# Kernel optimization log

Measured on AMD Instinct MI355X. Metric: run time of the kernel, lower is better.

## Reference

```python
import jax, jax.numpy as jnp
import numpy as np

B, N, D = 1, 4301, 768          # batch, tokens (4200 patch + 1 cls + 100 det), dim
H, HD = 12, 64                  # heads, head_dim (all_head_dim = 768)
NDET = 100                      # det tokens at the end of the sequence
EPS = 1e-5                      # torch LayerNorm default eps
SCALE = HD ** -0.5


def setup_inputs() -> dict:
    key = jax.random.key(0)
    ks = jax.random.split(key, 10)
    w = lambda k: jax.random.normal(k, (D, D), dtype=jnp.float32) * 0.02
    return {
        "x": jax.random.normal(ks[0], (B, N, D), dtype=jnp.float32),
        "wq_p": w(ks[1]), "wk_p": w(ks[2]), "wv_p": w(ks[3]),
        "wq_d": w(ks[4]), "wk_d": w(ks[5]), "wv_d": w(ks[6]),
        "bq_p": jnp.zeros((D,), jnp.float32), "bv_p": jnp.zeros((D,), jnp.float32),
        "bq_d": jnp.zeros((D,), jnp.float32), "bv_d": jnp.zeros((D,), jnp.float32),
        "ln_g": jnp.ones((D,), jnp.float32), "ln_b": jnp.zeros((D,), jnp.float32),
        "wo_p": w(ks[7]), "bo_p": jnp.zeros((D,), jnp.float32),
        "wo_d": w(ks[8]), "bo_d": jnp.zeros((D,), jnp.float32),
    }


def reference(x, wq_p, wk_p, wv_p, wq_d, wk_d, wv_d,
              bq_p, bv_p, bq_d, bv_d, ln_g, ln_b,
              wo_p, bo_p, wo_d, bo_d):
    xp = x[:, :-NDET, :]                       # [B, N-100, D] patch (+cls) tokens
    xd = x[:, -NDET:, :]                       # [B, 100, D]   det tokens
    # separate patch/det QKV projections (subln=True path; k has no bias)
    q = jnp.concatenate([xp @ wq_p.T + bq_p, xd @ wq_d.T + bq_d], axis=1)
    k = jnp.concatenate([xp @ wk_p.T,        xd @ wk_d.T],        axis=1)
    v = jnp.concatenate([xp @ wv_p.T + bv_p, xd @ wv_d.T + bv_d], axis=1)
    split = lambda t: t.reshape(B, N, H, HD).transpose(0, 2, 1, 3)  # [B,H,N,HD]
    q, k, v = split(q) * SCALE, split(k), split(v)
    # unfused attention (memory_efficient_attention_pytorch, attn_mask=None)
    attn = jax.nn.softmax(jnp.einsum("bhqd,bhkd->bhqk", q, k), axis=-1)
    o = jnp.einsum("bhqk,bhkd->bhqd", attn, v)
    o = o.transpose(0, 2, 1, 3).reshape(B, N, D)
    # inner_attn_ln (LayerNorm over all_head_dim)
    mu = o.mean(-1, keepdims=True)
    var = ((o - mu) ** 2).mean(-1, keepdims=True)
    o = (o - mu) * jax.lax.rsqrt(var + EPS) * ln_g + ln_b
    # separate patch/det output projections
    out = jnp.concatenate([o[:, :-NDET, :] @ wo_p.T + bo_p,
                           o[:, -NDET:, :] @ wo_d.T + bo_d], axis=1)
    return out
```

## Files before the change

kernel.cpp:

```cpp
#include <hip/hip_runtime.h>
#include <hip/hip_bf16.h>

#define NT 4301
#define NP 4201
#define NDET 100
#define DMODEL 768
#define NHEAD 12
#define HD 64
#define LN_EPS 1e-5f
#define LOG2E 1.4426950408889634f
#define QSCALE (0.125f * LOG2E)
#define NTP 4352
#define NCHUNK 68
#define FRAGSZ 512
#define CHUNKSZ 4096

typedef __hip_bfloat16 bf16;
typedef __attribute__((ext_vector_type(4))) float f32x4;
typedef __attribute__((ext_vector_type(8))) short frag8;
typedef __attribute__((ext_vector_type(2))) unsigned int u32x2;

static __device__ __forceinline__ void permlane32_swap(unsigned& a, unsigned& b) {
#if __has_builtin(__builtin_amdgcn_permlane32_swap)
    u32x2 r = __builtin_amdgcn_permlane32_swap(a, b, false, false);
    a = r[0]; b = r[1];
#else
    asm("v_permlane32_swap_b32 %0, %1" : "+v"(a), "+v"(b));
#endif
}
static __device__ __forceinline__ void permlane16_swap(unsigned& a, unsigned& b) {
#if __has_builtin(__builtin_amdgcn_permlane16_swap)
    u32x2 r = __builtin_amdgcn_permlane16_swap(a, b, false, false);
    a = r[0]; b = r[1];
#else
    asm("v_permlane16_swap_b32 %0, %1" : "+v"(a), "+v"(b));
#endif
}

static __device__ __forceinline__ unsigned pack_bf16_rh(float a, float b) {
    unsigned ua = __builtin_bit_cast(unsigned, a) + 0x8000u;
    unsigned ub = __builtin_bit_cast(unsigned, b) + 0x8000u;
    return __builtin_amdgcn_perm(ub, ua, 0x07060302u);
}

static __device__ __forceinline__ void gload16(const bf16* g, bf16* l) {
    __builtin_amdgcn_global_load_lds(
        (const __attribute__((address_space(1))) void*)g,
        (__attribute__((address_space(3))) void*)l, 16, 0, 0);
}

__global__ __launch_bounds__(256) void cast_all_kernel(
    const float* __restrict__ x,
    const float* __restrict__ w0, const float* __restrict__ w1,
    const float* __restrict__ w2, const float* __restrict__ w3,
    const float* __restrict__ w4, const float* __restrict__ w5,
    const float* __restrict__ w6, const float* __restrict__ w7,
    bf16* __restrict__ dst, int nx, int nw, int total) {
    int i4 = (blockIdx.x * 256 + threadIdx.x) * 4;
    if (i4 >= total) return;
    const float* s;
    int off;
    if (i4 < nx) {
        s = x; off = i4;
    } else {
        int r = i4 - nx;
        int w = r / nw;
        off = r - w * nw;
        s = w0;
        if (w == 1) s = w1; else if (w == 2) s = w2; else if (w == 3) s = w3;
        else if (w == 4) s = w4; else if (w == 5) s = w5;
        else if (w == 6) s = w6; else if (w == 7) s = w7;
    }
    float4 v = *(const float4*)(s + off);
    bf16 o[4] = {__float2bfloat16(v.x), __float2bfloat16(v.y),
                 __float2bfloat16(v.z), __float2bfloat16(v.w)};
    *(ushort4*)(dst + i4) = *(ushort4*)o;
}

__global__ __launch_bounds__(256, 4) void qkv_kernel(
    const bf16* __restrict__ xb, const bf16* __restrict__ wbase,
    const float* __restrict__ bq_p, const float* __restrict__ bq_d,
    const float* __restrict__ bv_p, const float* __restrict__ bv_d,
    bf16* __restrict__ Qb, bf16* __restrict__ Ksw, bf16* __restrict__ Vsw) {
    __shared__ bf16 As[64][32];
    __shared__ bf16 Bs[192][32];

    const int tid = threadIdx.x;
    const int wave = tid >> 6, lane = tid & 63;
    const int quad = lane >> 4, l16 = lane & 15;
    const int bx = blockIdx.x;
    const int h = blockIdx.y;
    const int is_det = bx >= 66;
    const int row0 = is_det ? NP + (bx - 66) * 64 : bx * 64;
    const int Mlim = is_det ? NT : NP;
    const int col0 = h * 64;
    const size_t nw = (size_t)DMODEL * DMODEL;
    const bf16* W = wbase + (is_det ? 3 * nw : 0);

    const f32x4 z4 = {0.f, 0.f, 0.f, 0.f};
    f32x4 acc[4][3];
#pragma unroll
    for (int r4 = 0; r4 < 4; ++r4)
#pragma unroll
        for (int f = 0; f < 3; ++f) acc[r4][f] = z4;

    const int srow = tid >> 2;
    const int scol8 = (tid & 3) * 8;
    int a_r = row0 + srow;
    if (a_r >= Mlim) a_r = Mlim - 1;
    const bf16* ap = xb + (size_t)a_r * DMODEL + scol8;
    const bf16* bp = W + (size_t)(col0 + srow) * DMODEL + scol8;

    uint4 areg  = *(const uint4*)(ap);
    uint4 breg0 = *(const uint4*)(bp);
    uint4 breg1 = *(const uint4*)(bp + nw);
    uint4 breg2 = *(const uint4*)(bp + 2 * nw);

    for (int k0 = 0; k0 < DMODEL; k0 += 32) {
        __syncthreads();
        *(uint4*)(&As[srow][scol8]) = areg;
        *(uint4*)(&Bs[srow][scol8]) = breg0;
        *(uint4*)(&Bs[64 + srow][scol8]) = breg1;
        *(uint4*)(&Bs[128 + srow][scol8]) = breg2;
        if (k0 + 32 < DMODEL) {
            areg  = *(const uint4*)(ap + k0 + 32);
            breg0 = *(const uint4*)(bp + k0 + 32);
            breg1 = *(const uint4*)(bp + nw + k0 + 32);
            breg2 = *(const uint4*)(bp + 2 * nw + k0 + 32);
        }
        __asm__ volatile("s_waitcnt lgkmcnt(0)" ::: "memory");
        __builtin_amdgcn_s_barrier();
        __asm__ volatile("" ::: "memory");
        frag8 af[4], bfr[3];
#pragma unroll
        for (int r4 = 0; r4 < 4; ++r4)
            af[r4] = *(const frag8*)(&As[r4 * 16 + l16][quad * 8]);
#pragma unroll
        for (int f = 0; f < 3; ++f)
            bfr[f] = *(const frag8*)(&Bs[wave * 48 + f * 16 + l16][quad * 8]);
#pragma unroll
        for (int r4 = 0; r4 < 4; ++r4)
#pragma unroll
            for (int f = 0; f < 3; ++f)
                acc[r4][f] = __builtin_amdgcn_mfma_f32_16x16x32_bf16(af[r4], bfr[f], acc[r4][f], 0, 0, 0);
        __asm__ volatile("" ::: "memory");
    }

#pragma unroll
    for (int f = 0; f < 3; ++f) {
        const int oc = 3 * wave + f;
        const int opi = oc >> 2;
        const int cin = (oc & 3) * 16 + l16;
        const int c = col0 + cin;
        float bv = 0.f, scale = 1.f;
        if (opi == 0) { bv = (is_det ? bq_d : bq_p)[c]; scale = QSCALE; }
        else if (opi == 2) { bv = (is_det ? bv_d : bv_p)[c]; }
#pragma unroll
        for (int r4 = 0; r4 < 4; ++r4) {
#pragma unroll
            for (int j = 0; j < 4; ++j) {
                const int r = row0 + r4 * 16 + quad * 4 + j;
                if (r >= Mlim) continue;
                const bf16 val = __float2bfloat16((acc[r4][f][j] + bv) * scale);
                if (opi == 0) {
                    Qb[(size_t)r * DMODEL + c] = val;
                } else if (opi == 1) {
                    const int cc = r >> 6, tf = (r >> 4) & 3, ln = r & 15;
                    const int s = cin >> 5, qd = (cin >> 3) & 3, je = cin & 7;
                    Ksw[((size_t)(h * NCHUNK + cc) * 8 + tf * 2 + s) * FRAGSZ +
                        (qd * 16 + ln) * 8 + je] = val;
                } else {
                    const int t = cin >> 4, le = cin & 15;
                    const int cc = r >> 6, rr = r & 63;
                    const int sv = rr >> 5, qv = (rr >> 3) & 3, je = rr & 7;
                    Vsw[((size_t)(h * NCHUNK + cc) * 8 + t * 2 + sv) * FRAGSZ +
                        (qv * 16 + le) * 8 + je] = val;
                }
            }
        }
    }
}

__global__ __launch_bounds__(256, 2) void attn_kernel(
    const bf16* __restrict__ Q, const bf16* __restrict__ Ksw,
    const bf16* __restrict__ Vsw, float* __restrict__ O_part,
    float* __restrict__ l_part, int cpb) {
    __shared__ bf16 KV[2][16][FRAGSZ];

    const int tid = threadIdx.x;
    const int wave = tid >> 6, lane = tid & 63;
    const int quad = lane >> 4, l16 = lane & 15;

    int bx, h, z;
    {
        const int id = blockIdx.x;
        const int nblk = gridDim.x;
        const int per = nblk >> 3;
        if ((nblk & 7) == 0 && per % 34 == 0) {
            const int ppx = per / 34;
            const int q = id >> 3;
            const int pair = (id & 7) * ppx + q / 34;
            bx = q % 34;
            h = pair % NHEAD; z = pair / NHEAD;
        } else {
            bx = id % 34; h = (id / 34) % NHEAD; z = id / (34 * NHEAD);
        }
    }
    const int qbase = bx * 128;
    const int hoff = h * HD;
    const int c0 = z * cpb, c1 = c0 + cpb;

    frag8 ones;
#pragma unroll
    for (int j = 0; j < 8; ++j) ones[j] = (short)0x3F80;

    frag8 qf[2][2];
#pragma unroll
    for (int g = 0; g < 2; ++g) {
        int qr = qbase + wave * 32 + g * 16 + l16;
        if (qr >= NT) qr = NT - 1;
#pragma unroll
        for (int s = 0; s < 2; ++s)
            qf[g][s] = *(const frag8*)(Q + (size_t)qr * DMODEL + hoff + s * 32 + quad * 8);
    }

    const bf16* kb0 = Ksw + (size_t)h * NCHUNK * CHUNKSZ + lane * 8;
    const bf16* vb0 = Vsw + (size_t)h * NCHUNK * CHUNKSZ + lane * 8;
    const bf16* sb = (wave < 2) ? kb0 : vb0;
    const int foff = (wave & 1) * 4;
    const int fbase = 4 * wave;

    const f32x4 z4 = {0.f, 0.f, 0.f, 0.f};
    f32x4 accO[2][4], accL[2];
#pragma unroll
    for (int g = 0; g < 2; ++g) {
        accL[g] = z4;
#pragma unroll
        for (int t = 0; t < 4; ++t) accO[g][t] = z4;
    }

    __asm__ volatile("s_waitcnt vmcnt(0)" ::: "memory");

    {
        const bf16* s = sb + (size_t)c0 * CHUNKSZ + foff * FRAGSZ;
#pragma unroll
        for (int i = 0; i < 4; ++i)
            gload16(s + i * FRAGSZ, &KV[0][fbase + i][0]);
    }

    int p = 0;
    for (int c = c0; c < c1; ++c) {
        if (c + 1 < c1) {
            const bf16* s = sb + (size_t)(c + 1) * CHUNKSZ + foff * FRAGSZ;
#pragma unroll
            for (int i = 0; i < 4; ++i)
                gload16(s + i * FRAGSZ, &KV[p ^ 1][fbase + i][0]);
            __asm__ volatile("s_waitcnt vmcnt(4)" ::: "memory");
        } else {
            __asm__ volatile("s_waitcnt vmcnt(0)" ::: "memory");
        }
        __builtin_amdgcn_s_barrier();
        __asm__ volatile("" ::: "memory");

        frag8 kf[8], vf[8];
#pragma unroll
        for (int f = 0; f < 8; ++f) {
            kf[f] = *(const frag8*)(&KV[p][f][lane * 8]);
            vf[f] = *(const frag8*)(&KV[p][8 + f][lane * 8]);
        }

        f32x4 S[2][4];
#pragma unroll
        for (int g = 0; g < 2; ++g)
#pragma unroll
            for (int t = 0; t < 4; ++t) {
                f32x4 s0 = __builtin_amdgcn_mfma_f32_16x16x32_bf16(kf[t * 2 + 0], qf[g][0], z4, 0, 0, 0);
                S[g][t]  = __builtin_amdgcn_mfma_f32_16x16x32_bf16(kf[t * 2 + 1], qf[g][1], s0, 0, 0, 0);
            }
        if (c == NCHUNK - 1) {
            const int kb = c * 64 + quad * 4;
#pragma unroll
            for (int t = 0; t < 4; ++t)
#pragma unroll
                for (int j = 0; j < 4; ++j)
                    if (kb + t * 16 + j >= NT) {
                        S[0][t][j] = -1e30f;
                        S[1][t][j] = -1e30f;
                    }
        }

#pragma unroll
        for (int g = 0; g < 2; ++g) {
            unsigned lo[4], hi[4];
#pragma unroll
            for (int t = 0; t < 4; ++t) {
                lo[t] = pack_bf16_rh(__builtin_exp2f(S[g][t][0]),
                                     __builtin_exp2f(S[g][t][1]));
                hi[t] = pack_bf16_rh(__builtin_exp2f(S[g][t][2]),
                                     __builtin_exp2f(S[g][t][3]));
            }
#pragma unroll
            for (int s = 0; s < 2; ++s) {
                unsigned A = lo[2 * s], B = hi[2 * s];
                unsigned C = lo[2 * s + 1], D = hi[2 * s + 1];
                permlane32_swap(A, C);
                permlane32_swap(B, D);
                permlane16_swap(A, C);
                permlane16_swap(B, D);
                union { unsigned u[4]; frag8 f; } pu;
                pu.u[0] = A; pu.u[1] = B; pu.u[2] = C; pu.u[3] = D;
                const frag8 pf = pu.f;
                accL[g] = __builtin_amdgcn_mfma_f32_16x16x32_bf16(pf, ones, accL[g], 0, 0, 0);
#pragma unroll
                for (int t = 0; t < 4; ++t)
                    accO[g][t] = __builtin_amdgcn_mfma_f32_16x16x32_bf16(pf, vf[t * 2 + s], accO[g][t], 0, 0, 0);
            }
        }

        __asm__ volatile("s_waitcnt lgkmcnt(0)" ::: "memory");
        __builtin_amdgcn_s_barrier();
        __asm__ volatile("" ::: "memory");
        p ^= 1;
    }

    float* Op = O_part + (size_t)z * NT * DMODEL;
#pragma unroll
    for (int g = 0; g < 2; ++g)
#pragma unroll
        for (int j = 0; j < 4; ++j) {
            const int r = qbase + wave * 32 + g * 16 + quad * 4 + j;
            if (r < NT) {
#pragma unroll
                for (int t = 0; t < 4; ++t)
                    Op[(size_t)r * DMODEL + hoff + t * 16 + l16] = accO[g][t][j];
                if (l16 == 0)
                    l_part[((size_t)z * NHEAD + h) * NTP + r] = accL[g][j];
            }
        }
}

__global__ __launch_bounds__(192) void reduce_ln_kernel(
    const float* __restrict__ O_part, const float* __restrict__ l_part,
    const float* __restrict__ g, const float* __restrict__ b,
    bf16* __restrict__ out, int nsplit) {
    const int n = blockIdx.x;
    const int tid = threadIdx.x;
    const int d0 = tid * 4;
    const int hh = d0 >> 6;

    float4 o = make_float4(0.f, 0.f, 0.f, 0.f);
    float lv = 0.f;
    for (int s = 0; s < nsplit; ++s) {
        float4 v = *(const float4*)(O_part + ((size_t)s * NT + n) * DMODEL + d0);
        o.x += v.x; o.y += v.y; o.z += v.z; o.w += v.w;
        lv += l_part[((size_t)s * NHEAD + hh) * NTP + n];
    }
    const float inv_l = 1.0f / lv;
    float vals[4] = {o.x * inv_l, o.y * inv_l, o.z * inv_l, o.w * inv_l};

    float s = vals[0] + vals[1] + vals[2] + vals[3];
    float s2 = vals[0] * vals[0] + vals[1] * vals[1] + vals[2] * vals[2] + vals[3] * vals[3];
#pragma unroll
    for (int off = 1; off < 64; off <<= 1) {
        s += __shfl_xor(s, off);
        s2 += __shfl_xor(s2, off);
    }
    __shared__ float ss[3], ss2[3];
    const int wave = tid >> 6, lane = tid & 63;
    if (lane == 0) { ss[wave] = s; ss2[wave] = s2; }
    __syncthreads();
    s = ss[0] + ss[1] + ss[2];
    s2 = ss2[0] + ss2[1] + ss2[2];
    const float mu = s * (1.0f / 768.0f);
    float var = s2 * (1.0f / 768.0f) - mu * mu;
    const float inv = rsqrtf(var + LN_EPS);

    unsigned short pk[4];
#pragma unroll
    for (int i = 0; i < 4; ++i) {
        const int d = d0 + i;
        const float v = (vals[i] - mu) * inv * g[d] + b[d];
        bf16 bb = __float2bfloat16(v);
        pk[i] = *(unsigned short*)&bb;
    }
    *(ushort4*)(out + (size_t)n * DMODEL + d0) = *(ushort4*)pk;
}

__global__ __launch_bounds__(256, 2) void out_kernel(
    const bf16* __restrict__ Lb, const bf16* __restrict__ wo,
    const float* __restrict__ bo_p, const float* __restrict__ bo_d,
    float* __restrict__ out) {
    __shared__ bf16 As[128][32];
    __shared__ bf16 Bs[64][32];

    const int tid = threadIdx.x;
    const int wave = tid >> 6, lane = tid & 63;
    const int quad = lane >> 4, l16 = lane & 15;
    const int bx = blockIdx.x;
    const int is_det = bx >= 33;
    const int row0 = is_det ? NP : bx * 128;
    const int Mlim = is_det ? NT : NP;
    const int col0 = blockIdx.y * 64;
    const size_t nw = (size_t)DMODEL * DMODEL;
    const bf16* B = wo + (is_det ? nw : 0);
    const float* bias = is_det ? bo_d : bo_p;

    const f32x4 z4 = {0.f, 0.f, 0.f, 0.f};
    f32x4 acc[2][4];
#pragma unroll
    for (int gg = 0; gg < 2; ++gg)
#pragma unroll
        for (int t = 0; t < 4; ++t) acc[gg][t] = z4;

    const int arow = tid >> 1;
    const int acol = (tid & 1) * 16;
    int a_r = row0 + arow;
    if (a_r >= Mlim) a_r = Mlim - 1;
    const bf16* ap = Lb + (size_t)a_r * DMODEL + acol;
    const int brow = tid >> 2;
    const int bcol = (tid & 3) * 8;
    const bf16* bp = B + (size_t)(col0 + brow) * DMODEL + bcol;

    uint4 areg0 = *(const uint4*)(ap);
    uint4 areg1 = *(const uint4*)(ap + 8);
    uint4 breg  = *(const uint4*)(bp);

    for (int k0 = 0; k0 < DMODEL; k0 += 32) {
        __syncthreads();
        *(uint4*)(&As[arow][acol]) = areg0;
        *(uint4*)(&As[arow][acol + 8]) = areg1;
        *(uint4*)(&Bs[brow][bcol]) = breg;
        if (k0 + 32 < DMODEL) {
            areg0 = *(const uint4*)(ap + k0 + 32);
            areg1 = *(const uint4*)(ap + k0 + 40);
            breg  = *(const uint4*)(bp + k0 + 32);
        }
        __asm__ volatile("s_waitcnt lgkmcnt(0)" ::: "memory");
        __builtin_amdgcn_s_barrier();
        __asm__ volatile("" ::: "memory");
        frag8 af[2], bfq[4];
#pragma unroll
        for (int gg = 0; gg < 2; ++gg)
            af[gg] = *(const frag8*)(&As[wave * 32 + gg * 16 + l16][quad * 8]);
#pragma unroll
        for (int t = 0; t < 4; ++t)
            bfq[t] = *(const frag8*)(&Bs[t * 16 + l16][quad * 8]);
#pragma unroll
        for (int gg = 0; gg < 2; ++gg)
#pragma unroll
            for (int t = 0; t < 4; ++t)
                acc[gg][t] = __builtin_amdgcn_mfma_f32_16x16x32_bf16(af[gg], bfq[t], acc[gg][t], 0, 0, 0);
        __asm__ volatile("" ::: "memory");
    }

#pragma unroll
    for (int gg = 0; gg < 2; ++gg) {
        const int rbase = row0 + wave * 32 + gg * 16 + quad * 4;
#pragma unroll
        for (int t = 0; t < 4; ++t) {
            const int c = col0 + t * 16 + l16;
            const float bv = bias[c];
#pragma unroll
            for (int j = 0; j < 4; ++j) {
                const int r = rbase + j;
                if (r < Mlim) out[(size_t)r * DMODEL + c] = acc[gg][t][j] + bv;
            }
        }
    }
}

extern "C" void kernel_launch(void* const* d_in, const int* in_sizes, int n_in,
                              void* d_out, int out_size, void* d_ws, size_t ws_size,
                              hipStream_t stream) {
    const float* x    = (const float*)d_in[0];
    const float* wq_p = (const float*)d_in[1];
    const float* wk_p = (const float*)d_in[2];
    const float* wv_p = (const float*)d_in[3];
    const float* wq_d = (const float*)d_in[4];
    const float* wk_d = (const float*)d_in[5];
    const float* wv_d = (const float*)d_in[6];
    const float* bq_p = (const float*)d_in[7];
    const float* bv_p = (const float*)d_in[8];
    const float* bq_d = (const float*)d_in[9];
    const float* bv_d = (const float*)d_in[10];
    const float* ln_g = (const float*)d_in[11];
    const float* ln_b = (const float*)d_in[12];
    const float* wo_p = (const float*)d_in[13];
    const float* bo_p = (const float*)d_in[14];
    const float* wo_d = (const float*)d_in[15];
    const float* bo_d = (const float*)d_in[16];
    float* out = (float*)d_out;

    const size_t nx  = (size_t)NT * DMODEL;
    const size_t nsw = (size_t)NHEAD * NCHUNK * CHUNKSZ;
    const size_t nw  = (size_t)DMODEL * DMODEL;

    char* ws = (char*)d_ws;
    bf16* xb   = (bf16*)ws; ws += nx * 2;
    bf16* wqkv = (bf16*)ws; ws += 6 * nw * 2;
    bf16* wob  = (bf16*)ws; ws += 2 * nw * 2;
    bf16* Qb   = (bf16*)ws; ws += nx * 2;
    bf16* Ksw  = (bf16*)ws; ws += nsw * 2;
    bf16* Vsw  = (bf16*)ws; ws += nsw * 2;
    const size_t fixed = (size_t)(ws - (char*)d_ws);

    const size_t per_split = nx * 4 + (size_t)NHEAD * NTP * 4;
    int nsplit = 1;
    if (ws_size >= fixed + 4 * per_split) nsplit = 4;
    else if (ws_size >= fixed + 2 * per_split) nsplit = 2;
    const int cpb = NCHUNK / nsplit;

    float* O_part = (float*)ws;
    float* l_part = (float*)(ws + (size_t)nsplit * nx * 4);
    bf16* Lb = xb;

    const int total = (int)(nx + 8 * nw);
    cast_all_kernel<<<dim3((total / 4 + 255) / 256), dim3(256), 0, stream>>>(
        x, wq_p, wk_p, wv_p, wq_d, wk_d, wv_d, wo_p, wo_d, xb, (int)nx, (int)nw, total);

    qkv_kernel<<<dim3(68, 12), dim3(256), 0, stream>>>(
        xb, wqkv, bq_p, bq_d, bv_p, bv_d, Qb, Ksw, Vsw);

    attn_kernel<<<dim3(34 * NHEAD * nsplit), dim3(256), 0, stream>>>(
        Qb, Ksw, Vsw, O_part, l_part, cpb);

    reduce_ln_kernel<<<dim3(NT), dim3(192), 0, stream>>>(
        O_part, l_part, ln_g, ln_b, Lb, nsplit);

    out_kernel<<<dim3(34, 12), dim3(256), 0, stream>>>(Lb, wob, bo_p, bo_d, out);
}
```

Before: 266.2 us.

## Raise attention occupancy by streaming K/V fragments from LDS and using native exp2

The launch-bounds occupancy hint for the attention kernel goes from 2 to 4 blocks per CU. To fit the tighter register budget, K and V fragments are no longer held all at once in registers but read from LDS just before the MFMAs that use them. The P·V loop is reordered so each V fragment is loaded once and used for both query groups. exp2 is switched to the hardware intrinsic. The risks are extra LDS reads interleaved with the MFMAs and possible register spills under the tighter bound.

After: 239.6 us. 10.0% less time.

```diff
diff --git a/kernel.cpp b/kernel.cpp
--- a/kernel.cpp
+++ b/kernel.cpp
@@ -34,6 +34,14 @@
     a = r[0]; b = r[1];
 #else
     asm("v_permlane16_swap_b32 %0, %1" : "+v"(a), "+v"(b));
+#endif
+}
+
+static __device__ __forceinline__ float fast_exp2(float x) {
+#if __has_builtin(__builtin_amdgcn_exp2f)
+    return __builtin_amdgcn_exp2f(x);
+#else
+    return __builtin_exp2f(x);
 #endif
 }
 
@@ -181,7 +189,7 @@
     }
 }
 
-__global__ __launch_bounds__(256, 2) void attn_kernel(
+__global__ __launch_bounds__(256, 4) void attn_kernel(
     const bf16* __restrict__ Q, const bf16* __restrict__ Ksw,
     const bf16* __restrict__ Vsw, float* __restrict__ O_part,
     float* __restrict__ l_part, int cpb) {
@@ -262,21 +270,17 @@
         __builtin_amdgcn_s_barrier();
         __asm__ volatile("" ::: "memory");
 
-        frag8 kf[8], vf[8];
-#pragma unroll
-        for (int f = 0; f < 8; ++f) {
-            kf[f] = *(const frag8*)(&KV[p][f][lane * 8]);
-            vf[f] = *(const frag8*)(&KV[p][8 + f][lane * 8]);
-        }
-
         f32x4 S[2][4];
 #pragma unroll
-        for (int g = 0; g < 2; ++g)
-#pragma unroll
-            for (int t = 0; t < 4; ++t) {
-                f32x4 s0 = __builtin_amdgcn_mfma_f32_16x16x32_bf16(kf[t * 2 + 0], qf[g][0], z4, 0, 0, 0);
-                S[g][t]  = __builtin_amdgcn_mfma_f32_16x16x32_bf16(kf[t * 2 + 1], qf[g][1], s0, 0, 0, 0);
-            }
+        for (int t = 0; t < 4; ++t) {
+            const frag8 k0 = *(const frag8*)(&KV[p][t * 2 + 0][lane * 8]);
+            const frag8 k1 = *(const frag8*)(&KV[p][t * 2 + 1][lane * 8]);
+#pragma unroll
+            for (int g = 0; g < 2; ++g) {
+                f32x4 s0 = __builtin_amdgcn_mfma_f32_16x16x32_bf16(k0, qf[g][0], z4, 0, 0, 0);
+                S[g][t]  = __builtin_amdgcn_mfma_f32_16x16x32_bf16(k1, qf[g][1], s0, 0, 0, 0);
+            }
+        }
         if (c == NCHUNK - 1) {
             const int kb = c * 64 + quad * 4;
 #pragma unroll
@@ -289,15 +293,14 @@
                     }
         }
 
+        frag8 pf[2][2];
 #pragma unroll
         for (int g = 0; g < 2; ++g) {
             unsigned lo[4], hi[4];
 #pragma unroll
             for (int t = 0; t < 4; ++t) {
-                lo[t] = pack_bf16_rh(__builtin_exp2f(S[g][t][0]),
-                                     __builtin_exp2f(S[g][t][1]));
-                hi[t] = pack_bf16_rh(__builtin_exp2f(S[g][t][2]),
-                                     __builtin_exp2f(S[g][t][3]));
+                lo[t] = pack_bf16_rh(fast_exp2(S[g][t][0]), fast_exp2(S[g][t][1]));
+                hi[t] = pack_bf16_rh(fast_exp2(S[g][t][2]), fast_exp2(S[g][t][3]));
             }
 #pragma unroll
             for (int s = 0; s < 2; ++s) {
@@ -309,13 +312,20 @@
                 permlane16_swap(B, D);
                 union { unsigned u[4]; frag8 f; } pu;
                 pu.u[0] = A; pu.u[1] = B; pu.u[2] = C; pu.u[3] = D;
-                const frag8 pf = pu.f;
-                accL[g] = __builtin_amdgcn_mfma_f32_16x16x32_bf16(pf, ones, accL[g], 0, 0, 0);
-#pragma unroll
-                for (int t = 0; t < 4; ++t)
-                    accO[g][t] = __builtin_amdgcn_mfma_f32_16x16x32_bf16(pf, vf[t * 2 + s], accO[g][t], 0, 0, 0);
-            }
-        }
+                pf[g][s] = pu.f;
+                accL[g] = __builtin_amdgcn_mfma_f32_16x16x32_bf16(pf[g][s], ones, accL[g], 0, 0, 0);
+            }
+        }
+
+#pragma unroll
+        for (int s = 0; s < 2; ++s)
+#pragma unroll
+            for (int t = 0; t < 4; ++t) {
+                const frag8 v = *(const frag8*)(&KV[p][8 + t * 2 + s][lane * 8]);
+#pragma unroll
+                for (int g = 0; g < 2; ++g)
+                    accO[g][t] = __builtin_amdgcn_mfma_f32_16x16x32_bf16(pf[g][s], v, accO[g][t], 0, 0, 0);
+            }
 
         __asm__ volatile("s_waitcnt lgkmcnt(0)" ::: "memory");
         __builtin_amdgcn_s_barrier();
```
